# Kernel tuning notes

Hardware: AMD Instinct MI355X
Metric: run time of the kernel (lower is better)

Reference implementation:

```python
import jax, jax.numpy as jnp
import numpy as np

N_NODES = 60000
N_HERB = 5000
N_PROT = 20000
PROT_OFFSET = N_HERB  # proteins follow herbs in the flattened node ordering
DIM = 128
N_REL = 6
N_BASES = 30
N_EDGES = 600000
N_PAIRS = 40000
HIDDEN = DIM


def setup_inputs() -> dict:
    key = jax.random.key(0)
    ks = jax.random.split(key, 16)
    inp = {}
    inp["edge_index"] = jax.random.randint(ks[0], (2, N_EDGES), 0, N_NODES)
    inp["edge_type"] = jax.random.randint(ks[1], (N_EDGES,), 0, N_REL)
    inp["h_idx"] = jax.random.randint(ks[2], (N_PAIRS,), 0, N_HERB)
    inp["p_idx"] = jax.random.randint(ks[3], (N_PAIRS,), 0, N_PROT)
    # learned node embeddings (all node types use nn.Embedding here)
    inp["node_emb"] = jax.random.normal(ks[4], (N_NODES, DIM), jnp.float32) * 0.1
    # RGCN layer 1 (basis decomposition + root + bias, as in PyG RGCNConv)
    inp["basis1"] = jax.random.normal(ks[5], (N_BASES, DIM, DIM), jnp.float32) * 0.05
    inp["comp1"] = jax.random.normal(ks[6], (N_REL, N_BASES), jnp.float32) * 0.1
    inp["root1"] = jax.random.normal(ks[7], (DIM, DIM), jnp.float32) * 0.05
    inp["bias1"] = jnp.zeros((DIM,), jnp.float32)
    # RGCN layer 2
    inp["basis2"] = jax.random.normal(ks[8], (N_BASES, DIM, DIM), jnp.float32) * 0.05
    inp["comp2"] = jax.random.normal(ks[9], (N_REL, N_BASES), jnp.float32) * 0.1
    inp["root2"] = jax.random.normal(ks[10], (DIM, DIM), jnp.float32) * 0.05
    inp["bias2"] = jnp.zeros((DIM,), jnp.float32)
    # scorer MLP: Linear(4*dim, hidden) -> ReLU -> Linear(hidden, 1)
    inp["sw1"] = jax.random.normal(ks[11], (4 * DIM, HIDDEN), jnp.float32) * 0.05
    inp["sb1"] = jnp.zeros((HIDDEN,), jnp.float32)
    inp["sw2"] = jax.random.normal(ks[12], (HIDDEN, 1), jnp.float32) * 0.05
    inp["sb2"] = jnp.zeros((1,), jnp.float32)
    return inp


def _rgcn_layer(x, edge_index, edge_type, basis, comp, root, bias):
    """PyG RGCNConv with basis decomposition, aggr='mean', root weight + bias.

    out[i] = sum_r mean_{j in N_r(i)} x_j @ W_r + x_i @ root + bias,
    with W_r = sum_b comp[r,b] * basis[b]. Because messages are linear, we
    aggregate (mean) per (dst, relation) first, then apply W_r once per node.
    """
    N, D = x.shape
    R = comp.shape[0]
    src, dst = edge_index[0], edge_index[1]
    seg = dst * R + edge_type  # segment per (destination, relation)
    sums = jax.ops.segment_sum(x[src], seg, num_segments=N * R)       # [N*R, D]
    cnt = jax.ops.segment_sum(jnp.ones_like(edge_type, dtype=x.dtype), seg,
                              num_segments=N * R)                      # [N*R]
    mean = (sums / jnp.maximum(cnt, 1.0)[:, None]).reshape(N, R, D)    # [N, R, D]
    W = jnp.einsum('rb,bdo->rdo', comp, basis)                         # [R, D, D]
    out = jnp.einsum('nrd,rdo->no', mean, W)
    return out + x @ root + bias


def reference(edge_index, edge_type, h_idx, p_idx, node_emb,
              basis1, comp1, root1, bias1,
              basis2, comp2, root2, bias2,
              sw1, sb1, sw2, sb2):
    x = _rgcn_layer(node_emb, edge_index, edge_type, basis1, comp1, root1, bias1)
    x = jax.nn.relu(x)
    # dropout omitted (eval mode)
    x = _rgcn_layer(x, edge_index, edge_type, basis2, comp2, root2, bias2)
    h = x[h_idx]                       # herbs occupy global ids [0, N_HERB)
    p = x[PROT_OFFSET + p_idx]         # proteins follow herbs
    feat = jnp.concatenate([h, p, h * p, jnp.abs(h - p)], axis=-1)  # [P, 4D]
    hid = jax.nn.relu(feat @ sw1 + sb1)
    return (hid @ sw2 + sb2).reshape(-1)
```

## Files before the change

### kernel.cpp

```cpp
#include <hip/hip_runtime.h>
#include <hip/hip_bf16.h>
#include <cstdint>

#define DIMX   128
#define N_REL  6
#define N_BASES 30
#define N_HERB 5000
#define NWIDE  896
#define YW     768
#define KSC    512
#define BN     64
#define KT     16

typedef __attribute__((ext_vector_type(8))) short short8v;
typedef __attribute__((ext_vector_type(4))) float f32x4;

__device__ __forceinline__ unsigned short f2bf_rne(float f) {
    union { float f; unsigned u; } v; v.f = f;
    unsigned u = v.u;
    u += 0x7fffu + ((u >> 16) & 1u);
    return (unsigned short)(u >> 16);
}
__device__ __forceinline__ float bf2f(unsigned short h) {
    union { unsigned u; float f; } v; v.u = ((unsigned)h) << 16;
    return v.f;
}


__global__ void k_count(const int* __restrict__ ei, const int* __restrict__ et,
                        int E, int* __restrict__ cnt) {
    int e = blockIdx.x * blockDim.x + threadIdx.x;
    if (e >= E) return;
    int dst = ei[E + e];
    int t   = et[e];
    atomicAdd(&cnt[dst * N_REL + t], 1);
}

__global__ void k_invcnt(const int* __restrict__ cnt, float* __restrict__ inv, int n) {
    int i = blockIdx.x * blockDim.x + threadIdx.x;
    if (i >= n) return;
    int c = cnt[i];
    inv[i] = 1.0f / (float)(c > 0 ? c : 1);
}

__global__ void k_deg(const int* __restrict__ cnt, int* __restrict__ deg, int n) {
    int i = blockIdx.x * blockDim.x + threadIdx.x;
    if (i >= n) return;
    int s = 0;
    #pragma unroll
    for (int t = 0; t < N_REL; ++t) s += cnt[i * N_REL + t];
    deg[i] = s;
}


__global__ void k_scan1(const int* __restrict__ deg, int* __restrict__ bsums, int n) {
    __shared__ int ssum[256];
    int tid = threadIdx.x;
    int base = blockIdx.x * 1024;
    int local = 0;
    #pragma unroll
    for (int i = 0; i < 4; ++i) {
        int idx = base + tid * 4 + i;
        local += (idx < n) ? deg[idx] : 0;
    }
    ssum[tid] = local; __syncthreads();
    for (int off = 128; off; off >>= 1) {
        if (tid < off) ssum[tid] += ssum[tid + off];
        __syncthreads();
    }
    if (tid == 0) bsums[blockIdx.x] = ssum[0];
}

__global__ void k_scan2(int* __restrict__ bsums, int nb, int* __restrict__ rowptr, int n) {
    if (threadIdx.x == 0 && blockIdx.x == 0) {
        int run = 0;
        for (int b = 0; b < nb; ++b) { int t = bsums[b]; bsums[b] = run; run += t; }
        rowptr[n] = run;
    }
}

__global__ void k_scan3(const int* __restrict__ deg, const int* __restrict__ bsums,
                        int* __restrict__ rowptr, int n) {
    __shared__ int ssum[256];
    int tid = threadIdx.x;
    int base = blockIdx.x * 1024;
    int idx0 = base + tid * 4;
    int v[4]; int local = 0;
    #pragma unroll
    for (int i = 0; i < 4; ++i) {
        int idx = idx0 + i;
        v[i] = (idx < n) ? deg[idx] : 0;
        local += v[i];
    }
    ssum[tid] = local; __syncthreads();
    for (int off = 1; off < 256; off <<= 1) {
        int t = (tid >= off) ? ssum[tid - off] : 0;
        __syncthreads();
        ssum[tid] += t;
        __syncthreads();
    }
    int excl = ssum[tid] - local + bsums[blockIdx.x];
    #pragma unroll
    for (int i = 0; i < 4; ++i) {
        int idx = idx0 + i;
        if (idx < n) { rowptr[idx] = excl; excl += v[i]; }
    }
}

__global__ void k_fill(const int* __restrict__ ei, const int* __restrict__ et, int E,
                       const int* __restrict__ rowptr, int* __restrict__ fillc,
                       int* __restrict__ pedge) {
    int e = blockIdx.x * blockDim.x + threadIdx.x;
    if (e >= E) return;
    int src = ei[e];
    int dst = ei[E + e];
    int t   = et[e];
    int pos = atomicAdd(&fillc[dst], 1);
    pedge[rowptr[dst] + pos] = (src << 3) | t;
}


__global__ void k_buildW2(const float* __restrict__ basis, const float* __restrict__ comp,
                          const float* __restrict__ root, unsigned short* __restrict__ W2) {
    int d = blockIdx.x;
    int r = blockIdx.y;
    int o = threadIdx.x;
    float v;
    if (r < N_REL) {
        float acc = 0.f;
        #pragma unroll
        for (int b = 0; b < N_BASES; ++b)
            acc += comp[r * N_BASES + b] * basis[((size_t)b * DIMX + d) * DIMX + o];
        v = acc;
    } else {
        v = root[(size_t)d * DIMX + o];
    }
    unsigned short hi = f2bf_rne(v);
    unsigned short lo = f2bf_rne(v - bf2f(hi));
    size_t og = (size_t)(r * DIMX + o);
    W2[og * 256 + d] = hi;
    W2[og * 256 + 128 + d] = lo;
}


__global__ __launch_bounds__(256)
void k_prepA(const float* __restrict__ x, unsigned short* __restrict__ A2,
             int NN, int relu) {
    int row = blockIdx.x * 16 + (threadIdx.x >> 4);
    int c8  = (threadIdx.x & 15) * 8;
    float v[8];
    bool ok = (row < NN);
    if (ok) {
        float4 a = *(const float4*)(x + (size_t)row * DIMX + c8);
        float4 b = *(const float4*)(x + (size_t)row * DIMX + c8 + 4);
        v[0]=a.x; v[1]=a.y; v[2]=a.z; v[3]=a.w;
        v[4]=b.x; v[5]=b.y; v[6]=b.z; v[7]=b.w;
        if (relu) {
            #pragma unroll
            for (int i = 0; i < 8; ++i) v[i] = fmaxf(v[i], 0.f);
        }
    }
    __syncthreads();
    if (ok) {
        unsigned short hi[8], lo[8];
        #pragma unroll
        for (int i = 0; i < 8; ++i) {
            hi[i] = f2bf_rne(v[i]);
            lo[i] = f2bf_rne(v[i] - bf2f(hi[i]));
        }
        unsigned short* base = A2 + (size_t)row * 256;
        *(ulonglong2*)(base + c8)       = *(ulonglong2*)hi;
        *(ulonglong2*)(base + 128 + c8) = *(ulonglong2*)lo;
    }
}


__global__ __launch_bounds__(256)
void k_gemm_mfma(const unsigned short* __restrict__ A2, const unsigned short* __restrict__ W2,
                 const float* __restrict__ bias, float* __restrict__ y,
                 float* __restrict__ outbuf, int NN) {
    int tid = threadIdx.x;
    int w  = tid >> 6;
    int l  = tid & 63;
    int cl = l & 15;
    int kg = (l >> 4) * 8;
    int cb = blockIdx.y;
    int rowBase = blockIdx.x * 64;
    if (rowBase >= NN) return;
    int nt = (NN - rowBase) >> 4; if (nt > 4) nt = 4;

    int ocol0 = w * 32;
    const unsigned short* bB0 = W2 + (size_t)(cb * DIMX + ocol0 + cl) * 256 + kg;
    const unsigned short* bB1 = bB0 + 16 * 256;

    short8v b0h[4], b0l[4], b1h[4], b1l[4];
    #pragma unroll
    for (int k0 = 0; k0 < 4; ++k0) {
        b0h[k0] = *(const short8v*)(bB0 + k0 * 32);
        b0l[k0] = *(const short8v*)(bB0 + 128 + k0 * 32);
        b1h[k0] = *(const short8v*)(bB1 + k0 * 32);
        b1l[k0] = *(const short8v*)(bB1 + 128 + k0 * 32);
    }

    int rq = (l >> 4) * 4;

    for (int t = 0; t < nt; ++t) {
        int r0 = rowBase + t * 16;
        const unsigned short* aB = A2 + (size_t)(r0 + cl) * 256 + kg;
        f32x4 acc0 = (f32x4){0.f, 0.f, 0.f, 0.f};
        f32x4 acc1 = (f32x4){0.f, 0.f, 0.f, 0.f};
        #pragma unroll
        for (int k0 = 0; k0 < 4; ++k0) {
            short8v ah = *(const short8v*)(aB + k0 * 32);
            short8v al = *(const short8v*)(aB + 128 + k0 * 32);
            acc0 = __builtin_amdgcn_mfma_f32_16x16x32_bf16(ah, b0h[k0], acc0, 0, 0, 0);
            acc0 = __builtin_amdgcn_mfma_f32_16x16x32_bf16(al, b0h[k0], acc0, 0, 0, 0);
            acc0 = __builtin_amdgcn_mfma_f32_16x16x32_bf16(ah, b0l[k0], acc0, 0, 0, 0);
            acc1 = __builtin_amdgcn_mfma_f32_16x16x32_bf16(ah, b1h[k0], acc1, 0, 0, 0);
            acc1 = __builtin_amdgcn_mfma_f32_16x16x32_bf16(al, b1h[k0], acc1, 0, 0, 0);
            acc1 = __builtin_amdgcn_mfma_f32_16x16x32_bf16(ah, b1l[k0], acc1, 0, 0, 0);
        }
        if (cb < N_REL) {
            float* yb = y + (size_t)(r0 + rq) * YW + cb * DIMX + ocol0 + cl;
            #pragma unroll
            for (int q = 0; q < 4; ++q) {
                yb[(size_t)q * YW]      = acc0[q];
                yb[(size_t)q * YW + 16] = acc1[q];
            }
        } else {
            float bv0 = bias[ocol0 + cl];
            float bv1 = bias[ocol0 + 16 + cl];
            float* ob = outbuf + (size_t)(r0 + rq) * DIMX + ocol0 + cl;
            #pragma unroll
            for (int q = 0; q < 4; ++q) {
                ob[(size_t)q * DIMX]      = acc0[q] + bv0;
                ob[(size_t)q * DIMX + 16] = acc1[q] + bv1;
            }
        }
    }
}


__global__ __launch_bounds__(256)
void k_gather(const int* __restrict__ pedge, const int* __restrict__ rowptr,
              const float* __restrict__ invc, const float* __restrict__ y,
              float* __restrict__ outbuf, int NN) {
    int wid = (blockIdx.x * blockDim.x + threadIdx.x) >> 6;
    if (wid >= NN) return;
    int lane = threadIdx.x & 63;
    int dst = wid;
    int j0 = rowptr[dst], j1 = rowptr[dst + 1];

    float* op = outbuf + (size_t)dst * DIMX + lane * 2;
    float2 acc = *(float2*)op;

    int j = j0;
    for (; j + 1 < j1; j += 2) {
        int pa = pedge[j], pb = pedge[j + 1];
        int ta = pa & 7, tb = pb & 7;
        int sa = pa >> 3, sb = pb >> 3;
        float fa = invc[dst * N_REL + ta];
        float fb = invc[dst * N_REL + tb];
        float2 va = *(const float2*)(y + (size_t)sa * YW + ta * DIMX + lane * 2);
        float2 vb = *(const float2*)(y + (size_t)sb * YW + tb * DIMX + lane * 2);
        acc.x += va.x * fa + vb.x * fb;
        acc.y += va.y * fa + vb.y * fb;
    }
    if (j < j1) {
        int pa = pedge[j];
        int ta = pa & 7;
        int sa = pa >> 3;
        float fa = invc[dst * N_REL + ta];
        float2 va = *(const float2*)(y + (size_t)sa * YW + ta * DIMX + lane * 2);
        acc.x += va.x * fa;
        acc.y += va.y * fa;
    }
    *(float2*)op = acc;
}


__global__ __launch_bounds__(256)
void k_scorer_gemm(const float* __restrict__ x2, const int* __restrict__ h_idx,
                   const int* __restrict__ p_idx, const float* __restrict__ sw1,
                   const float* __restrict__ sb1, float* __restrict__ hid, int P) {
    __shared__ float As[BN][KT];
    __shared__ float Ws[KT][DIMX];
    int tid = threadIdx.x;
    int n0 = blockIdx.x * BN;

    int lrow = tid >> 2;
    int lk4  = (tid & 3) * 4;
    int ng = n0 + lrow; if (ng >= P) ng = P - 1;
    int hrow = h_idx[ng];
    int prow = N_HERB + p_idx[ng];

    int oc = (tid & 31) * 4;
    int nb = (tid >> 5) * 8;

    float acc[8][4];
    #pragma unroll
    for (int i = 0; i < 8; ++i)
        #pragma unroll
        for (int j = 0; j < 4; ++j) acc[i][j] = 0.f;

    for (int k0 = 0; k0 < KSC; k0 += KT) {
        int k = k0 + lk4;
        int q = k >> 7;
        int d = k & 127;
        float4 hv = *(const float4*)(x2 + (size_t)hrow * DIMX + d);
        float4 pv = *(const float4*)(x2 + (size_t)prow * DIMX + d);
        float4 av;
        if (q == 0)      av = hv;
        else if (q == 1) av = pv;
        else if (q == 2) { av.x = hv.x * pv.x; av.y = hv.y * pv.y;
                           av.z = hv.z * pv.z; av.w = hv.w * pv.w; }
        else             { av.x = fabsf(hv.x - pv.x); av.y = fabsf(hv.y - pv.y);
                           av.z = fabsf(hv.z - pv.z); av.w = fabsf(hv.w - pv.w); }
        *(float4*)&As[lrow][lk4] = av;

        const float4* wsrc = (const float4*)(sw1 + (size_t)k0 * DIMX);
        ((float4*)Ws)[tid]       = wsrc[tid];
        ((float4*)Ws)[tid + 256] = wsrc[tid + 256];
        __syncthreads();

        #pragma unroll
        for (int kk = 0; kk < KT; kk += 4) {
            float4 wv0 = *(float4*)&Ws[kk + 0][oc];
            float4 wv1 = *(float4*)&Ws[kk + 1][oc];
            float4 wv2 = *(float4*)&Ws[kk + 2][oc];
            float4 wv3 = *(float4*)&Ws[kk + 3][oc];
            #pragma unroll
            for (int i = 0; i < 8; ++i) {
                float4 a4 = *(float4*)&As[nb + i][kk];
                acc[i][0] += a4.x * wv0.x + a4.y * wv1.x + a4.z * wv2.x + a4.w * wv3.x;
                acc[i][1] += a4.x * wv0.y + a4.y * wv1.y + a4.z * wv2.y + a4.w * wv3.y;
                acc[i][2] += a4.x * wv0.z + a4.y * wv1.z + a4.z * wv2.z + a4.w * wv3.z;
                acc[i][3] += a4.x * wv0.w + a4.y * wv1.w + a4.z * wv2.w + a4.w * wv3.w;
            }
        }
        __syncthreads();
    }

    float4 bv = *(const float4*)(sb1 + oc);
    #pragma unroll
    for (int i = 0; i < 8; ++i) {
        int n = n0 + nb + i;
        if (n < P) {
            float4 r;
            r.x = fmaxf(acc[i][0] + bv.x, 0.f);
            r.y = fmaxf(acc[i][1] + bv.y, 0.f);
            r.z = fmaxf(acc[i][2] + bv.z, 0.f);
            r.w = fmaxf(acc[i][3] + bv.w, 0.f);
            *(float4*)(hid + (size_t)n * DIMX + oc) = r;
        }
    }
}


__global__ void k_scorer_out(const float* __restrict__ hid, const float* __restrict__ sw2,
                             const float* __restrict__ sb2, float* __restrict__ out, int P) {
    int tid = blockIdx.x * blockDim.x + threadIdx.x;
    int wave = tid >> 6;
    int lane = tid & 63;
    int half = lane >> 5, l32 = lane & 31;
    int pair = wave * 2 + half;
    if (pair >= P) return;
    float4 hv = *(const float4*)(hid + (size_t)pair * DIMX + l32 * 4);
    float4 wv = *(const float4*)(sw2 + l32 * 4);
    float s = hv.x * wv.x + hv.y * wv.y + hv.z * wv.z + hv.w * wv.w;
    #pragma unroll
    for (int off = 16; off; off >>= 1) s += __shfl_xor(s, off, 64);
    if (l32 == 0) out[pair] = s + sb2[0];
}


extern "C" void kernel_launch(void* const* d_in, const int* in_sizes, int n_in,
                              void* d_out, int out_size, void* d_ws, size_t ws_size,
                              hipStream_t stream) {
    const int*   ei       = (const int*)d_in[0];
    const int*   et       = (const int*)d_in[1];
    const int*   h_idx    = (const int*)d_in[2];
    const int*   p_idx    = (const int*)d_in[3];
    const float* node_emb = (const float*)d_in[4];
    const float* basis1   = (const float*)d_in[5];
    const float* comp1    = (const float*)d_in[6];
    const float* root1    = (const float*)d_in[7];
    const float* bias1    = (const float*)d_in[8];
    const float* basis2   = (const float*)d_in[9];
    const float* comp2    = (const float*)d_in[10];
    const float* root2    = (const float*)d_in[11];
    const float* bias2    = (const float*)d_in[12];
    const float* sw1      = (const float*)d_in[13];
    const float* sb1      = (const float*)d_in[14];
    const float* sw2      = (const float*)d_in[15];
    const float* sb2      = (const float*)d_in[16];
    float* out = (float*)d_out;

    int E  = in_sizes[1];
    int P  = in_sizes[2];
    int NN = in_sizes[4] / DIMX;

    float* y      = (float*)d_ws;
    float* hid    = y;
    int*   cnt    = (int*)(y + (size_t)NN * YW);
    float* invc   = (float*)(cnt + (size_t)NN * N_REL);
    float* out1   = invc + (size_t)NN * N_REL;
    float* out2   = out1 + (size_t)NN * DIMX;
    unsigned short* W2 = (unsigned short*)(out2 + (size_t)NN * DIMX);
    int*   deg    = (int*)(W2 + (size_t)NWIDE * 256);
    int*   rowptr = deg + NN;
    int*   fillc  = rowptr + NN + 1;
    int*   bsums  = fillc + NN;
    int*   pedge  = bsums + 64;

    unsigned short* A2_l1 = (unsigned short*)out2;
    unsigned short* A2_l2 = (unsigned short*)out1;

    int nScanB = (NN + 1023) / 1024;

    hipMemsetAsync(cnt, 0, (size_t)NN * N_REL * sizeof(int), stream);
    hipMemsetAsync(fillc, 0, (size_t)NN * sizeof(int), stream);

    k_count<<<(E + 255) / 256, 256, 0, stream>>>(ei, et, E, cnt);
    k_invcnt<<<(NN * N_REL + 255) / 256, 256, 0, stream>>>(cnt, invc, NN * N_REL);
    k_deg<<<(NN + 255) / 256, 256, 0, stream>>>(cnt, deg, NN);
    k_scan1<<<nScanB, 256, 0, stream>>>(deg, bsums, NN);
    k_scan2<<<1, 64, 0, stream>>>(bsums, nScanB, rowptr, NN);
    k_scan3<<<nScanB, 256, 0, stream>>>(deg, bsums, rowptr, NN);
    k_fill<<<(E + 255) / 256, 256, 0, stream>>>(ei, et, E, rowptr, fillc, pedge);

    dim3 gemmGrid((NN + 63) / 64, N_REL + 1);
    dim3 wGrid(DIMX, N_REL + 1);
    int prepBlocks = (NN + 15) / 16;
    int gatherBlocks = ((size_t)NN * 64 + 255) / 256;

    k_buildW2<<<wGrid, DIMX, 0, stream>>>(basis1, comp1, root1, W2);
    k_prepA<<<prepBlocks, 256, 0, stream>>>(node_emb, A2_l1, NN, 0);
    k_gemm_mfma<<<gemmGrid, 256, 0, stream>>>(A2_l1, W2, bias1, y, out1, NN);
    k_gather<<<gatherBlocks, 256, 0, stream>>>(pedge, rowptr, invc, y, out1, NN);

    k_buildW2<<<wGrid, DIMX, 0, stream>>>(basis2, comp2, root2, W2);
    k_prepA<<<prepBlocks, 256, 0, stream>>>(out1, A2_l2, NN, 1);
    k_gemm_mfma<<<gemmGrid, 256, 0, stream>>>(A2_l2, W2, bias2, y, out2, NN);
    k_gather<<<gatherBlocks, 256, 0, stream>>>(pedge, rowptr, invc, y, out2, NN);

    k_scorer_gemm<<<(P + BN - 1) / BN, 256, 0, stream>>>(out2, h_idx, p_idx, sw1, sb1, hid, P);
    k_scorer_out<<<((size_t)P * 32 + 255) / 256, 256, 0, stream>>>(hid, sw2, sb2, out, P);
}
```

Before: 736.7 us.

## Store per-relation transformed features in bf16 and loop relations inside GEMM block

```diff
diff --git a/kernel.cpp b/kernel.cpp
--- a/kernel.cpp
+++ b/kernel.cpp
@@ -177,64 +177,65 @@
 
 __global__ __launch_bounds__(256)
 void k_gemm_mfma(const unsigned short* __restrict__ A2, const unsigned short* __restrict__ W2,
-                 const float* __restrict__ bias, float* __restrict__ y,
+                 const float* __restrict__ bias, unsigned short* __restrict__ y,
                  float* __restrict__ outbuf, int NN) {
     int tid = threadIdx.x;
     int w  = tid >> 6;
     int l  = tid & 63;
     int cl = l & 15;
     int kg = (l >> 4) * 8;
-    int cb = blockIdx.y;
     int rowBase = blockIdx.x * 64;
     if (rowBase >= NN) return;
     int nt = (NN - rowBase) >> 4; if (nt > 4) nt = 4;
 
     int ocol0 = w * 32;
-    const unsigned short* bB0 = W2 + (size_t)(cb * DIMX + ocol0 + cl) * 256 + kg;
-    const unsigned short* bB1 = bB0 + 16 * 256;
-
-    short8v b0h[4], b0l[4], b1h[4], b1l[4];
-    #pragma unroll
-    for (int k0 = 0; k0 < 4; ++k0) {
-        b0h[k0] = *(const short8v*)(bB0 + k0 * 32);
-        b0l[k0] = *(const short8v*)(bB0 + 128 + k0 * 32);
-        b1h[k0] = *(const short8v*)(bB1 + k0 * 32);
-        b1l[k0] = *(const short8v*)(bB1 + 128 + k0 * 32);
-    }
-
     int rq = (l >> 4) * 4;
-
-    for (int t = 0; t < nt; ++t) {
-        int r0 = rowBase + t * 16;
-        const unsigned short* aB = A2 + (size_t)(r0 + cl) * 256 + kg;
-        f32x4 acc0 = (f32x4){0.f, 0.f, 0.f, 0.f};
-        f32x4 acc1 = (f32x4){0.f, 0.f, 0.f, 0.f};
+    float bv0 = bias[ocol0 + cl];
+    float bv1 = bias[ocol0 + 16 + cl];
+
+    for (int cb = 0; cb < N_REL + 1; ++cb) {
+        const unsigned short* bB0 = W2 + (size_t)(cb * DIMX + ocol0 + cl) * 256 + kg;
+        const unsigned short* bB1 = bB0 + 16 * 256;
+
+        short8v b0h[4], b0l[4], b1h[4], b1l[4];
         #pragma unroll
         for (int k0 = 0; k0 < 4; ++k0) {
-            short8v ah = *(const short8v*)(aB + k0 * 32);
-            short8v al = *(const short8v*)(aB + 128 + k0 * 32);
-            acc0 = __builtin_amdgcn_mfma_f32_16x16x32_bf16(ah, b0h[k0], acc0, 0, 0, 0);
-            acc0 = __builtin_amdgcn_mfma_f32_16x16x32_bf16(al, b0h[k0], acc0, 0, 0, 0);
-            acc0 = __builtin_amdgcn_mfma_f32_16x16x32_bf16(ah, b0l[k0], acc0, 0, 0, 0);
-            acc1 = __builtin_amdgcn_mfma_f32_16x16x32_bf16(ah, b1h[k0], acc1, 0, 0, 0);
-            acc1 = __builtin_amdgcn_mfma_f32_16x16x32_bf16(al, b1h[k0], acc1, 0, 0, 0);
-            acc1 = __builtin_amdgcn_mfma_f32_16x16x32_bf16(ah, b1l[k0], acc1, 0, 0, 0);
-        }
-        if (cb < N_REL) {
-            float* yb = y + (size_t)(r0 + rq) * YW + cb * DIMX + ocol0 + cl;
+            b0h[k0] = *(const short8v*)(bB0 + k0 * 32);
+            b0l[k0] = *(const short8v*)(bB0 + 128 + k0 * 32);
+            b1h[k0] = *(const short8v*)(bB1 + k0 * 32);
+            b1l[k0] = *(const short8v*)(bB1 + 128 + k0 * 32);
+        }
+
+        for (int t = 0; t < nt; ++t) {
+            int r0 = rowBase + t * 16;
+            const unsigned short* aB = A2 + (size_t)(r0 + cl) * 256 + kg;
+            f32x4 acc0 = (f32x4){0.f, 0.f, 0.f, 0.f};
+            f32x4 acc1 = (f32x4){0.f, 0.f, 0.f, 0.f};
             #pragma unroll
-            for (int q = 0; q < 4; ++q) {
-                yb[(size_t)q * YW]      = acc0[q];
-                yb[(size_t)q * YW + 16] = acc1[q];
+            for (int k0 = 0; k0 < 4; ++k0) {
+                short8v ah = *(const short8v*)(aB + k0 * 32);
+                short8v al = *(const short8v*)(aB + 128 + k0 * 32);
+                acc0 = __builtin_amdgcn_mfma_f32_16x16x32_bf16(ah, b0h[k0], acc0, 0, 0, 0);
+                acc0 = __builtin_amdgcn_mfma_f32_16x16x32_bf16(al, b0h[k0], acc0, 0, 0, 0);
+                acc0 = __builtin_amdgcn_mfma_f32_16x16x32_bf16(ah, b0l[k0], acc0, 0, 0, 0);
+                acc1 = __builtin_amdgcn_mfma_f32_16x16x32_bf16(ah, b1h[k0], acc1, 0, 0, 0);
+                acc1 = __builtin_amdgcn_mfma_f32_16x16x32_bf16(al, b1h[k0], acc1, 0, 0, 0);
+                acc1 = __builtin_amdgcn_mfma_f32_16x16x32_bf16(ah, b1l[k0], acc1, 0, 0, 0);
             }
-        } else {
-            float bv0 = bias[ocol0 + cl];
-            float bv1 = bias[ocol0 + 16 + cl];
-            float* ob = outbuf + (size_t)(r0 + rq) * DIMX + ocol0 + cl;
-            #pragma unroll
-            for (int q = 0; q < 4; ++q) {
-                ob[(size_t)q * DIMX]      = acc0[q] + bv0;
-                ob[(size_t)q * DIMX + 16] = acc1[q] + bv1;
+            if (cb < N_REL) {
+                unsigned short* yb = y + (size_t)(r0 + rq) * YW + cb * DIMX + ocol0 + cl;
+                #pragma unroll
+                for (int q = 0; q < 4; ++q) {
+                    yb[(size_t)q * YW]      = f2bf_rne(acc0[q]);
+                    yb[(size_t)q * YW + 16] = f2bf_rne(acc1[q]);
+                }
+            } else {
+                float* ob = outbuf + (size_t)(r0 + rq) * DIMX + ocol0 + cl;
+                #pragma unroll
+                for (int q = 0; q < 4; ++q) {
+                    ob[(size_t)q * DIMX]      = acc0[q] + bv0;
+                    ob[(size_t)q * DIMX + 16] = acc1[q] + bv1;
+                }
             }
         }
     }
@@ -243,7 +244,7 @@
 
 __global__ __launch_bounds__(256)
 void k_gather(const int* __restrict__ pedge, const int* __restrict__ rowptr,
-              const float* __restrict__ invc, const float* __restrict__ y,
+              const float* __restrict__ invc, const unsigned short* __restrict__ y,
               float* __restrict__ outbuf, int NN) {
     int wid = (blockIdx.x * blockDim.x + threadIdx.x) >> 6;
     if (wid >= NN) return;
@@ -261,19 +262,21 @@
         int sa = pa >> 3, sb = pb >> 3;
         float fa = invc[dst * N_REL + ta];
         float fb = invc[dst * N_REL + tb];
-        float2 va = *(const float2*)(y + (size_t)sa * YW + ta * DIMX + lane * 2);
-        float2 vb = *(const float2*)(y + (size_t)sb * YW + tb * DIMX + lane * 2);
-        acc.x += va.x * fa + vb.x * fb;
-        acc.y += va.y * fa + vb.y * fb;
+        unsigned va = *(const unsigned*)(y + (size_t)sa * YW + ta * DIMX + lane * 2);
+        unsigned vb = *(const unsigned*)(y + (size_t)sb * YW + tb * DIMX + lane * 2);
+        acc.x += bf2f((unsigned short)(va & 0xffff)) * fa
+               + bf2f((unsigned short)(vb & 0xffff)) * fb;
+        acc.y += bf2f((unsigned short)(va >> 16)) * fa
+               + bf2f((unsigned short)(vb >> 16)) * fb;
     }
     if (j < j1) {
         int pa = pedge[j];
         int ta = pa & 7;
         int sa = pa >> 3;
         float fa = invc[dst * N_REL + ta];
-        float2 va = *(const float2*)(y + (size_t)sa * YW + ta * DIMX + lane * 2);
-        acc.x += va.x * fa;
-        acc.y += va.y * fa;
+        unsigned va = *(const unsigned*)(y + (size_t)sa * YW + ta * DIMX + lane * 2);
+        acc.x += bf2f((unsigned short)(va & 0xffff)) * fa;
+        acc.y += bf2f((unsigned short)(va >> 16)) * fa;
     }
     *(float2*)op = acc;
 }
@@ -400,9 +403,10 @@
     int P  = in_sizes[2];
     int NN = in_sizes[4] / DIMX;
 
-    float* y      = (float*)d_ws;
-    float* hid    = y;
-    int*   cnt    = (int*)(y + (size_t)NN * YW);
+    unsigned short* y = (unsigned short*)d_ws;
+    float* hid    = (float*)d_ws;
+    float* fbase  = (float*)(y + (size_t)NN * YW);
+    int*   cnt    = (int*)fbase;
     float* invc   = (float*)(cnt + (size_t)NN * N_REL);
     float* out1   = invc + (size_t)NN * N_REL;
     float* out2   = out1 + (size_t)NN * DIMX;
@@ -429,19 +433,19 @@
     k_scan3<<<nScanB, 256, 0, stream>>>(deg, bsums, rowptr, NN);
     k_fill<<<(E + 255) / 256, 256, 0, stream>>>(ei, et, E, rowptr, fillc, pedge);
 
-    dim3 gemmGrid((NN + 63) / 64, N_REL + 1);
+    int gemmBlocks = (NN + 63) / 64;
     dim3 wGrid(DIMX, N_REL + 1);
     int prepBlocks = (NN + 15) / 16;
     int gatherBlocks = ((size_t)NN * 64 + 255) / 256;
 
     k_buildW2<<<wGrid, DIMX, 0, stream>>>(basis1, comp1, root1, W2);
     k_prepA<<<prepBlocks, 256, 0, stream>>>(node_emb, A2_l1, NN, 0);
-    k_gemm_mfma<<<gemmGrid, 256, 0, stream>>>(A2_l1, W2, bias1, y, out1, NN);
+    k_gemm_mfma<<<gemmBlocks, 256, 0, stream>>>(A2_l1, W2, bias1, y, out1, NN);
     k_gather<<<gatherBlocks, 256, 0, stream>>>(pedge, rowptr, invc, y, out1, NN);
 
     k_buildW2<<<wGrid, DIMX, 0, stream>>>(basis2, comp2, root2, W2);
     k_prepA<<<prepBlocks, 256, 0, stream>>>(out1, A2_l2, NN, 1);
-    k_gemm_mfma<<<gemmGrid, 256, 0, stream>>>(A2_l2, W2, bias2, y, out2, NN);
+    k_gemm_mfma<<<gemmBlocks, 256, 0, stream>>>(A2_l2, W2, bias2, y, out2, NN);
     k_gather<<<gatherBlocks, 256, 0, stream>>>(pedge, rowptr, invc, y, out2, NN);
 
     k_scorer_gemm<<<(P + BN - 1) / BN, 256, 0, stream>>>(out2, h_idx, p_idx, sw1, sb1, hid, P);
```

Result: no change. 733.7 us (-0.4%).
